# Kernel tuning notes

Hardware: AMD Instinct MI355X
Metric: run time of the kernel (lower is better)

Reference implementation:

```python
import jax, jax.numpy as jnp
import numpy as np

NH, HD, MBS = 32, 64, 16   # num_heads, head_dim, mini_batch_size
BASE_LR = 1.0
ROPE_BASE = 10000.0
EPS = 1e-6


def _rotate_half(x):
    x1, x2 = jnp.split(x, 2, axis=-1)
    return jnp.concatenate((-x2, x1), axis=-1)


def _permute_qk(x):
    B, H, L, D = x.shape
    return x.reshape(B, H, L, D // 2, 2).swapaxes(-1, -2).reshape(B, H, L, D)


def _undo_permute_qk(x):
    B, H, L, D = x.shape
    return x.reshape(B, H, L, 2, D // 2).swapaxes(-1, -2).reshape(B, H, L, D)


def _ln_fwd(x, gamma, beta):
    mu = x.mean(-1, keepdims=True)
    var = x.var(-1, keepdims=True)
    return gamma * ((x - mu) / jnp.sqrt(var + EPS)) + beta


def _ln_fused_l2_bwd(x, target, gamma, beta):
    # grad of 0.5*||LN(x) - target||^2 wrt x, fused
    D = x.shape[-1]
    mu = x.mean(-1, keepdims=True)
    std = jnp.sqrt(x.var(-1, keepdims=True) + EPS)
    x_hat = (x - mu) / std
    y = gamma * x_hat + beta
    g = (y - target) * gamma
    return (D * g - g.sum(-1, keepdims=True) - x_hat * (g * x_hat).sum(-1, keepdims=True)) / (D * std)


def setup_inputs() -> dict:
    key = jax.random.key(0)
    ks = jax.random.split(key, 8)
    B, L, C, OUT = 4, 2048, 2048, 768
    s = 0.02
    return {
        "hidden_states": jax.random.normal(ks[0], (B, L, C), jnp.float32),
        "position_ids": jnp.broadcast_to(jnp.arange(L, dtype=jnp.int32)[None], (B, L)),
        "Wq": jax.random.normal(ks[1], (C, C), jnp.float32) * s,
        "Wk": jax.random.normal(ks[2], (C, C), jnp.float32) * s,
        "Wv": jax.random.normal(ks[3], (C, C), jnp.float32) * s,
        "Wo": jax.random.normal(ks[4], (C, OUT), jnp.float32) * s,
        "W1": jax.random.normal(ks[5], (NH, HD, HD), jnp.float32) * s,
        "b1": jnp.zeros((NH, 1, HD), jnp.float32),
        "ttt_lr_weight": jax.random.normal(ks[6], (NH, 1, C), jnp.float32) * s,
        "ttt_lr_bias": jnp.zeros((NH, 1), jnp.float32),
        "learnable_token_idx": jnp.zeros((MBS,), jnp.float32),
        "ttt_norm_weight": jnp.ones((NH, HD), jnp.float32),
        "ttt_norm_bias": jnp.zeros((NH, HD), jnp.float32),
        "post_norm_weight": jnp.ones((C,), jnp.float32),
        "post_norm_bias": jnp.zeros((C,), jnp.float32),
    }


def reference(hidden_states, position_ids, Wq, Wk, Wv, Wo, W1, b1,
              ttt_lr_weight, ttt_lr_bias, learnable_token_idx,
              ttt_norm_weight, ttt_norm_bias, post_norm_weight, post_norm_bias):
    B, L, C = hidden_states.shape
    NM = L // MBS
    # QKV projections -> [B, NH, L, HD]
    XQ = (hidden_states @ Wq).reshape(B, L, NH, HD).transpose(0, 2, 1, 3)
    XK = (hidden_states @ Wk).reshape(B, L, NH, HD).transpose(0, 2, 1, 3)
    XV = (hidden_states @ Wv).reshape(B, L, NH, HD).transpose(0, 2, 1, 3)
    # RoPE on positions modulo the mini-batch size
    pos = (position_ids % MBS).astype(jnp.float32)  # [B, L]
    inv_freq = 1.0 / (ROPE_BASE ** (jnp.arange(0, HD, 2, dtype=jnp.float32) / HD))
    freqs = pos[..., None] * inv_freq               # [B, L, HD/2]
    emb = jnp.concatenate((freqs, freqs), axis=-1)  # [B, L, HD]
    cos = jnp.cos(emb)[:, None]                     # [B, 1, L, HD]
    sin = jnp.sin(emb)[:, None]
    XQ, XK = _permute_qk(XQ), _permute_qk(XK)
    XQ = XQ * cos + _rotate_half(XQ) * sin
    XK = XK * cos + _rotate_half(XK) * sin
    XQ, XK = _undo_permute_qk(XQ), _undo_permute_qk(XK)
    # reshape into mini-batches: [B, NH, NM, K, HD]
    X = hidden_states.reshape(B, NM, MBS, C)
    XQ = XQ.reshape(B, NH, NM, MBS, HD)
    XK = XK.reshape(B, NH, NM, MBS, HD)
    XV = XV.reshape(B, NH, NM, MBS, HD)
    # eta: per-token learnable LR gate
    ttt_lr = jax.nn.sigmoid(
        jnp.einsum('bnkc,hdc->bhnkd', X, ttt_lr_weight)
        + ttt_lr_bias.reshape(1, NH, 1, 1, 1))              # [B,NH,NM,K,1]
    ttt_lr_eta = BASE_LR * ttt_lr.transpose(0, 1, 2, 4, 3) / HD  # [B,NH,NM,1,K]
    token_idx = jnp.clip(1.0 / jnp.arange(1, MBS + 1, dtype=jnp.float32)
                         + learnable_token_idx, 0.0, None)
    token_eta = token_idx.reshape(1, 1, 1, MBS, 1)
    eta = token_eta * ttt_lr_eta                            # [B,NH,NM,K,K]
    # TTT-Linear dual-form mini-batch scan
    ln_w = ttt_norm_weight.reshape(1, NH, 1, HD)
    ln_b = ttt_norm_bias.reshape(1, NH, 1, HD)
    W1_0 = jnp.broadcast_to(W1[None], (B, NH, HD, HD))
    b1_0 = jnp.broadcast_to(b1[None], (B, NH, 1, HD))
    tril = jnp.tril(jnp.ones((MBS, MBS), hidden_states.dtype))

    def step(carry, xs):
        W1_s, b1_s = carry
        xq, xk, xv, eta_m = xs                 # [B,NH,K,HD], eta_m [B,NH,K,K]
        Z1 = xk @ W1_s + b1_s
        target = xv - xk
        grad = _ln_fused_l2_bwd(Z1, target, ln_w, ln_b)
        Attn = tril * (xq @ xk.swapaxes(-1, -2))
        b1_bar = b1_s - (tril * eta_m) @ grad
        Z1_bar = xq @ W1_s - (eta_m * Attn) @ grad + b1_bar
        last_eta = eta_m[:, :, -1, :, None]    # [B,NH,K,1]
        W1_new = W1_s - (last_eta * xk).swapaxes(-1, -2) @ grad
        b1_new = b1_s - jnp.sum(last_eta * grad, axis=-2, keepdims=True)
        out = xq + _ln_fwd(Z1_bar, ln_w, ln_b)
        return (W1_new, b1_new), out

    xs = (XQ.transpose(2, 0, 1, 3, 4), XK.transpose(2, 0, 1, 3, 4),
          XV.transpose(2, 0, 1, 3, 4), eta.transpose(2, 0, 1, 3, 4))
    _, outs = jax.lax.scan(step, (W1_0, b1_0), xs)   # [NM,B,NH,K,HD]
    out = outs.transpose(1, 2, 0, 3, 4).reshape(B, NH, L, HD)
    out = out.transpose(0, 2, 1, 3).reshape(B, L, C)
    # post LayerNorm (eps 1e-6) and output projection
    mu = out.mean(-1, keepdims=True)
    var = out.var(-1, keepdims=True)
    out = (out - mu) / jnp.sqrt(var + EPS) * post_norm_weight + post_norm_bias
    return out @ Wo
```

## Files before the change

kernel.cpp:

```cpp
#include <hip/hip_runtime.h>
#include <cstddef>
#include <cstdint>

#define B_DIM   4
#define L_SEQ   2048
#define C_DIM   2048
#define OUT_DIM 768
#define NHEADS  32
#define HDIM    64
#define MBS_    16
#define NMINI   128
#define EPS_    1e-6f

typedef _Float16 half8 __attribute__((ext_vector_type(8)));
typedef float floatx4 __attribute__((ext_vector_type(4)));

__device__ __forceinline__ void glds16(const void* g, void* l) {
    __builtin_amdgcn_global_load_lds(
        (const __attribute__((address_space(1))) uint32_t*)g,
        (__attribute__((address_space(3))) uint32_t*)l, 16, 0, 0);
}

__device__ __forceinline__ void split8(const float4 a, const float4 b,
                                       half8& hi, half8& lo) {
    const float x[8] = {a.x, a.y, a.z, a.w, b.x, b.y, b.z, b.w};
#pragma unroll
    for (int e = 0; e < 8; e++) {
        const _Float16 h = (_Float16)x[e];
        hi[e] = h;
        lo[e] = (_Float16)(x[e] - (float)h);
    }
}

__global__ __launch_bounds__(256)
void gemm_af32(const float* __restrict__ A,
               const _Float16* __restrict__ Bhi, const _Float16* __restrict__ Blo,
               float* __restrict__ Cout, int mode, int doRope)
{
    __shared__ __align__(16) float    sA[4096];
    __shared__ __align__(16) _Float16 sBhi[4096];
    __shared__ __align__(16) _Float16 sBlo[4096];
    const int tid = threadIdx.x;
    const int m0 = blockIdx.y * 128, n0 = blockIdx.x * 128;
    const int K = 2048;

    size_t gA[4]; float* lA[4];
#pragma unroll
    for (int I = 0; I < 4; I++) {
        const int c = I * 256 + tid;
        const int row = c >> 3, seg = (c & 7) ^ (row & 7);
        gA[I] = (size_t)(m0 + row) * K + seg * 4;
        lA[I] = &sA[c * 4];
    }
    size_t gB[2]; _Float16 *lBh[2], *lBl[2];
#pragma unroll
    for (int I = 0; I < 2; I++) {
        const int c = I * 256 + tid;
        const int row = c >> 2, seg = (c & 3) ^ ((row >> 1) & 3);
        gB[I] = (size_t)(n0 + row) * K + seg * 8;
        lBh[I] = &sBhi[c * 8];
        lBl[I] = &sBlo[c * 8];
    }

    const int lane = tid & 63, quad = lane >> 4, lc = lane & 15;
    const int wv = tid >> 6, wm = wv & 1, wn = wv >> 1;
    int offA0[4], offA1[4], offB[4];
#pragma unroll
    for (int i = 0; i < 4; i++) {
        const int rA = wm * 64 + i * 16 + lc;
        offA0[i] = (rA * 8 + ((2 * quad)     ^ (rA & 7))) * 4;
        offA1[i] = (rA * 8 + ((2 * quad + 1) ^ (rA & 7))) * 4;
    }
#pragma unroll
    for (int j = 0; j < 4; j++) {
        const int rB = wn * 64 + j * 16 + lc;
        offB[j] = (rB * 4 + (quad ^ ((rB >> 1) & 3))) * 8;
    }

    floatx4 acc[4][4];
#pragma unroll
    for (int i = 0; i < 4; i++)
#pragma unroll
        for (int j = 0; j < 4; j++) acc[i][j] = (floatx4)0.0f;

    for (int k0 = 0; k0 < K; k0 += 32) {
        __syncthreads();
#pragma unroll
        for (int I = 0; I < 4; I++) glds16(A + gA[I] + k0, lA[I]);
#pragma unroll
        for (int I = 0; I < 2; I++) {
            glds16(Bhi + gB[I] + k0, lBh[I]);
            glds16(Blo + gB[I] + k0, lBl[I]);
        }
        __syncthreads();

        half8 ah[4], al[4], bh[4], bl[4];
#pragma unroll
        for (int i = 0; i < 4; i++) {
            const float4 va = *(const float4*)&sA[offA0[i]];
            const float4 vb = *(const float4*)&sA[offA1[i]];
            split8(va, vb, ah[i], al[i]);
        }
#pragma unroll
        for (int j = 0; j < 4; j++) {
            bh[j] = *(const half8*)&sBhi[offB[j]];
            bl[j] = *(const half8*)&sBlo[offB[j]];
        }
#pragma unroll
        for (int i = 0; i < 4; i++)
#pragma unroll
            for (int j = 0; j < 4; j++) {
                acc[i][j] = __builtin_amdgcn_mfma_f32_16x16x32_f16(ah[i], bh[j], acc[i][j], 0, 0, 0);
                acc[i][j] = __builtin_amdgcn_mfma_f32_16x16x32_f16(ah[i], bl[j], acc[i][j], 0, 0, 0);
                acc[i][j] = __builtin_amdgcn_mfma_f32_16x16x32_f16(al[i], bh[j], acc[i][j], 0, 0, 0);
            }
    }

    float cs[4][4], sn[4][4];
    if (doRope) {
#pragma unroll
        for (int j = 0; j < 4; j++) {
            const int ii = ((j * 16 + lc) & 63) >> 1;
            const float invf = expf(-(float)ii * 0.28782313662425574f);
#pragma unroll
            for (int r = 0; r < 4; r++) {
                const float ang = (float)(quad * 4 + r) * invf;
                sincosf(ang, &sn[j][r], &cs[j][r]);
            }
        }
    }
    const int oddcol = lc & 1;
#pragma unroll
    for (int i = 0; i < 4; i++) {
#pragma unroll
        for (int j = 0; j < 4; j++) {
            floatx4 v = acc[i][j];
            if (doRope) {
#pragma unroll
                for (int r = 0; r < 4; r++) {
                    const float partner = __shfl_xor(v[r], 1);
                    v[r] = v[r] * cs[j][r] + partner * (oddcol ? sn[j][r] : -sn[j][r]);
                }
            }
            const int n = n0 + wn * 64 + j * 16 + lc;
            if (mode == 0) {
                const int h = (n >> 6) & 31, d = n & 63;
#pragma unroll
                for (int r = 0; r < 4; r++) {
                    const int m = m0 + wm * 64 + i * 16 + quad * 4 + r;
                    const int b = m >> 11, li = m & 2047;
                    Cout[((size_t)(b * 32 + h) * 2048 + li) * 64 + d] = v[r];
                }
            } else {
#pragma unroll
                for (int r = 0; r < 4; r++) {
                    const int m = m0 + wm * 64 + i * 16 + quad * 4 + r;
                    Cout[(size_t)m * OUT_DIM + n] = v[r];
                }
            }
        }
    }
}

__global__ __launch_bounds__(256)
void wtrans_kernel(const float* __restrict__ W, _Float16* __restrict__ BThi,
                   _Float16* __restrict__ BTlo, int Nw)
{
    __shared__ float tile[32][33];
    const int t = threadIdx.x, tx = t & 31, ty = t >> 5;
    const int n0 = blockIdx.x * 32, k0 = blockIdx.y * 32;
    const int K = 2048;
#pragma unroll
    for (int r = 0; r < 4; r++)
        tile[ty + r * 8][tx] = W[(size_t)(k0 + ty + r * 8) * Nw + n0 + tx];
    __syncthreads();
#pragma unroll
    for (int r = 0; r < 4; r++) {
        const float val = tile[tx][ty + r * 8];
        const _Float16 hh = (_Float16)val;
        const size_t o = (size_t)(n0 + ty + r * 8) * K + k0 + tx;
        BThi[o] = hh;
        BTlo[o] = (_Float16)(val - (float)hh);
    }
}

__global__ __launch_bounds__(256)
void lr_kernel(const float* __restrict__ hidden, const float* __restrict__ wlr,
               const float* __restrict__ lr_bias, float* __restrict__ lrs)
{
    __shared__ float sRow[2048];
    __shared__ float sPart[32][9];
    const int m = blockIdx.x;
    const int t = threadIdx.x;
    const float* row = hidden + (size_t)m * C_DIM;
#pragma unroll
    for (int j = 0; j < 8; j++) sRow[t + j * 256] = row[t + j * 256];
    __syncthreads();
    const int h = t >> 3, p = t & 7;
    const float* w = wlr + (size_t)h * C_DIM;
    float s = 0.0f;
#pragma unroll 8
    for (int k = 0; k < 64; k++) {
        const int c = k * 32 + p * 4;
        const float4 a = *(const float4*)(sRow + c);
        const float4 b = *(const float4*)(w + c);
        s += a.x * b.x + a.y * b.y + a.z * b.z + a.w * b.w;
    }
    sPart[h][p] = s;
    __syncthreads();
    if (t < 32) {
        float v = 0.0f;
#pragma unroll
        for (int p2 = 0; p2 < 8; p2++) v += sPart[t][p2];
        v += lr_bias[t];
        const float sig = 1.0f / (1.0f + expf(-v));
        lrs[((size_t)(m >> 11) * NHEADS + t) * L_SEQ + (m & 2047)] = sig;
    }
}

__global__ __launch_bounds__(256, 1)
void scan_mfma(const float* __restrict__ XQ, const float* __restrict__ XK,
               float* __restrict__ XVo, const float* __restrict__ LRS,
               const float* __restrict__ W1i, const float* __restrict__ b1i,
               const float* __restrict__ lt, const float* __restrict__ lnw,
               const float* __restrict__ lnb)
{
    __shared__ __align__(16) float sXq[1024];
    __shared__ __align__(16) float sXk[1024];
    __shared__ __align__(16) float sXv[16 * 68];
    __shared__ __align__(16) float sW1T[4096];
    __shared__ __align__(16) float sGt[64 * 36];
    __shared__ __align__(16) float sKt[64 * 36];
    __shared__ __align__(16) float sCf[16 * 36];
    __shared__ __align__(16) float sRed[16 * 8];
    __shared__ float sMu[16], sRstd[16], sG1[16], sG2[16];
    __shared__ float sB1[64], sGam[64], sBet[64];
    __shared__ __align__(16) float sEta[32];
    __shared__ float sTok[16];

    const int bh = blockIdx.x, h = bh & 31;
    const int t = threadIdx.x;
    const int lane = t & 63, q = lane >> 4, lc = lane & 15;
    const int w = t >> 6;
    const int col = w * 16 + lc;
    const int iRow = t >> 4;
    const int c0 = (t & 15) * 4;
    const int cellP = (t & 15) ^ (iRow & 15);

    if (t < 64) { sB1[t] = b1i[h * 64 + t]; sGam[t] = lnw[h * 64 + t]; sBet[t] = lnb[h * 64 + t]; }
    if (t < 16) sTok[t] = fmaxf(1.0f / (float)(t + 1) + lt[t], 0.0f);
    if (t < 32) sEta[t] = 0.0f;
    for (int idx = t; idx < 1024; idx += 256) {
        const int r = idx >> 4, c = 16 + (idx & 15);
        sGt[r * 36 + c] = 0.0f;
        sKt[r * 36 + c] = 0.0f;
    }
    { const int r = t >> 4, c = 16 + (t & 15); sCf[r * 36 + c] = 0.0f; }

    float w1s[4][4];
#pragma unroll
    for (int t4 = 0; t4 < 4; t4++)
#pragma unroll
        for (int r = 0; r < 4; r++)
            w1s[t4][r] = W1i[h * 4096 + (16 * t4 + lc) * 64 + (16 * w + 4 * q + r)];
#pragma unroll
    for (int t4 = 0; t4 < 4; t4++)
#pragma unroll
        for (int r = 0; r < 4; r++) {
            const int nn = 16 * w + 4 * q + r, k = 16 * t4 + lc;
            sW1T[nn * 64 + ((((k >> 2) ^ (nn & 15)) << 2) | (k & 3))] = w1s[t4][r];
        }
    __syncthreads();

    const float tok15 = sTok[15];
    const float gamC = sGam[col], betC = sBet[col];
    float tokR[4];
#pragma unroll
    for (int r = 0; r < 4; r++) tokR[r] = sTok[4 * q + r];

    const size_t base = (size_t)bh * L_SEQ * HDIM;
    const float* xq_g = XQ + base;
    const float* xk_g = XK + base;
    float* xv_g = XVo + base;
    const float* lr_g = LRS + (size_t)bh * L_SEQ;

    float4 cq = *(const float4*)(xq_g + t * 4);
    float4 ck = *(const float4*)(xk_g + t * 4);
    float4 cv = *(const float4*)(xv_g + t * 4);
    float clr = lr_g[t & 15];

    for (int n = 0; n < NMINI; n++) {
        *(float4*)&sXq[iRow * 64 + (cellP << 2)] = cq;
        *(float4*)&sXk[iRow * 64 + (cellP << 2)] = ck;
        *(float4*)&sXv[iRow * 68 + c0] = cv;
        if (t < 16) sEta[t] = clr * (1.0f / 64.0f);
        const int np = (n + 1) & (NMINI - 1);
        const float4 nq = *(const float4*)(xq_g + np * 1024 + t * 4);
        const float4 nk = *(const float4*)(xk_g + np * 1024 + t * 4);
        const float4 nv = *(const float4*)(xv_g + np * 1024 + t * 4);
        const float nlr = lr_g[np * 16 + (t & 15)];
        __syncthreads();

        {
            const float le = tok15 * sEta[iRow];
            sKt[(c0 + 0) * 36 + iRow] = ck.x * le;
            sKt[(c0 + 1) * 36 + iRow] = ck.y * le;
            sKt[(c0 + 2) * 36 + iRow] = ck.z * le;
            sKt[(c0 + 3) * 36 + iRow] = ck.w * le;
        }

        half8 qh[2], ql[2], kh[2], kl[2], wh[2], wl[2];
#pragma unroll
        for (int f = 0; f < 2; f++) {
            const int ca = (8 * f + 2 * q) ^ lc, cb = (8 * f + 2 * q + 1) ^ lc;
            {
                const float4 u0 = *(const float4*)&sXq[lc * 64 + ca * 4];
                const float4 u1 = *(const float4*)&sXq[lc * 64 + cb * 4];
                split8(u0, u1, qh[f], ql[f]);
            }
            {
                const float4 u0 = *(const float4*)&sXk[lc * 64 + ca * 4];
                const float4 u1 = *(const float4*)&sXk[lc * 64 + cb * 4];
                split8(u0, u1, kh[f], kl[f]);
            }
            {
                const int rw = 16 * w + lc;
                const float4 u0 = *(const float4*)&sW1T[rw * 64 + ca * 4];
                const float4 u1 = *(const float4*)&sW1T[rw * 64 + cb * 4];
                split8(u0, u1, wh[f], wl[f]);
            }
        }

        floatx4 z1a = (floatx4)0.0f, zba = (floatx4)0.0f, at = (floatx4)0.0f;
#pragma unroll
        for (int f = 0; f < 2; f++) {
            z1a = __builtin_amdgcn_mfma_f32_16x16x32_f16(kh[f], wh[f], z1a, 0, 0, 0);
            z1a = __builtin_amdgcn_mfma_f32_16x16x32_f16(kh[f], wl[f], z1a, 0, 0, 0);
            z1a = __builtin_amdgcn_mfma_f32_16x16x32_f16(kl[f], wh[f], z1a, 0, 0, 0);
            zba = __builtin_amdgcn_mfma_f32_16x16x32_f16(qh[f], wh[f], zba, 0, 0, 0);
            zba = __builtin_amdgcn_mfma_f32_16x16x32_f16(qh[f], wl[f], zba, 0, 0, 0);
            zba = __builtin_amdgcn_mfma_f32_16x16x32_f16(ql[f], wh[f], zba, 0, 0, 0);
        }
        if (w == 0) {
#pragma unroll
            for (int f = 0; f < 2; f++) {
                at = __builtin_amdgcn_mfma_f32_16x16x32_f16(qh[f], kh[f], at, 0, 0, 0);
                at = __builtin_amdgcn_mfma_f32_16x16x32_f16(qh[f], kl[f], at, 0, 0, 0);
                at = __builtin_amdgcn_mfma_f32_16x16x32_f16(ql[f], kh[f], at, 0, 0, 0);
            }
        }

        const float b1c = sB1[col];
        float z[4], s1[4], s2[4];
#pragma unroll
        for (int r = 0; r < 4; r++) { z[r] = z1a[r] + b1c; s1[r] = z[r]; s2[r] = z[r] * z[r]; }
#pragma unroll
        for (int o = 1; o < 16; o <<= 1)
#pragma unroll
            for (int r = 0; r < 4; r++) { s1[r] += __shfl_xor(s1[r], o); s2[r] += __shfl_xor(s2[r], o); }
        if (lc == 0)
#pragma unroll
            for (int r = 0; r < 4; r++) {
                const int row = 4 * q + r;
                sRed[row * 8 + w] = s1[r];
                sRed[row * 8 + 4 + w] = s2[r];
            }
        __syncthreads();
        if (t < 16) {
            const float4 a = *(const float4*)&sRed[t * 8];
            const float4 b = *(const float4*)&sRed[t * 8 + 4];
            const float mu = (a.x + a.y + a.z + a.w) * (1.0f / 64.0f);
            const float ex2 = (b.x + b.y + b.z + b.w) * (1.0f / 64.0f);
            sMu[t] = mu;
            sRstd[t] = rsqrtf(ex2 - mu * mu + EPS_);
        }
        __syncthreads();

        float gg[4], xh[4];
#pragma unroll
        for (int r = 0; r < 4; r++) {
            const int row = 4 * q + r;
            const float mu = sMu[row], rs = sRstd[row];
            xh[r] = (z[r] - mu) * rs;
            const float xkv = sXk[row * 64 + (((((col >> 2) ^ row) & 15) << 2) | (col & 3))];
            const float tgt = sXv[row * 68 + col] - xkv;
            gg[r] = (gamC * xh[r] + betC - tgt) * gamC;
            s1[r] = gg[r]; s2[r] = gg[r] * xh[r];
        }
#pragma unroll
        for (int o = 1; o < 16; o <<= 1)
#pragma unroll
            for (int r = 0; r < 4; r++) { s1[r] += __shfl_xor(s1[r], o); s2[r] += __shfl_xor(s2[r], o); }
        if (lc == 0)
#pragma unroll
            for (int r = 0; r < 4; r++) {
                const int row = 4 * q + r;
                sRed[row * 8 + w] = s1[r];
                sRed[row * 8 + 4 + w] = s2[r];
            }
        __syncthreads();
        if (t < 16) {
            const float4 a = *(const float4*)&sRed[t * 8];
            const float4 b = *(const float4*)&sRed[t * 8 + 4];
            sG1[t] = a.x + a.y + a.z + a.w;
            sG2[t] = b.x + b.y + b.z + b.w;
        }
        __syncthreads();
#pragma unroll
        for (int r = 0; r < 4; r++) {
            const int row = 4 * q + r;
            const float rs = sRstd[row];
            const float gr = (64.0f * gg[r] - sG1[row] - xh[r] * sG2[row]) * rs * (1.0f / 64.0f);
            sGt[col * 36 + row] = gr;
        }
        if (w == 0) {
            const float ej = sEta[lc];
#pragma unroll
            for (int r = 0; r < 4; r++) {
                const int i = 4 * q + r;
                const float cf = (lc <= i) ? -tokR[r] * ej * (at[r] + 1.0f) : 0.0f;
                sCf[i * 36 + lc] = cf;
            }
        }
        __syncthreads();

        half8 cfh, cfl, gth, gtl;
        {
            const float4 u0 = *(const float4*)&sCf[lc * 36 + 8 * q];
            const float4 u1 = *(const float4*)&sCf[lc * 36 + 8 * q + 4];
            split8(u0, u1, cfh, cfl);
        }
        {
            const int rw = 16 * w + lc;
            const float4 u0 = *(const float4*)&sGt[rw * 36 + 8 * q];
            const float4 u1 = *(const float4*)&sGt[rw * 36 + 8 * q + 4];
            split8(u0, u1, gth, gtl);
        }
        zba = __builtin_amdgcn_mfma_f32_16x16x32_f16(cfh, gth, zba, 0, 0, 0);
        zba = __builtin_amdgcn_mfma_f32_16x16x32_f16(cfh, gtl, zba, 0, 0, 0);
        zba = __builtin_amdgcn_mfma_f32_16x16x32_f16(cfl, gth, zba, 0, 0, 0);
#pragma unroll
        for (int t4 = 0; t4 < 4; t4++) {
            half8 kth, ktl;
            const float4 u0 = *(const float4*)&sKt[(16 * t4 + lc) * 36 + 8 * q];
            const float4 u1 = *(const float4*)&sKt[(16 * t4 + lc) * 36 + 8 * q + 4];
            split8(u0, u1, kth, ktl);
            floatx4 up = (floatx4)0.0f;
            up = __builtin_amdgcn_mfma_f32_16x16x32_f16(gth, kth, up, 0, 0, 0);
            up = __builtin_amdgcn_mfma_f32_16x16x32_f16(gth, ktl, up, 0, 0, 0);
            up = __builtin_amdgcn_mfma_f32_16x16x32_f16(gtl, kth, up, 0, 0, 0);
#pragma unroll
            for (int r = 0; r < 4; r++) w1s[t4][r] -= up[r];
        }

        float z2[4];
#pragma unroll
        for (int r = 0; r < 4; r++) { z2[r] = zba[r] + b1c; s1[r] = z2[r]; s2[r] = z2[r] * z2[r]; }
#pragma unroll
        for (int o = 1; o < 16; o <<= 1)
#pragma unroll
            for (int r = 0; r < 4; r++) { s1[r] += __shfl_xor(s1[r], o); s2[r] += __shfl_xor(s2[r], o); }
        if (lc == 0)
#pragma unroll
            for (int r = 0; r < 4; r++) {
                const int row = 4 * q + r;
                sRed[row * 8 + w] = s1[r];
                sRed[row * 8 + 4 + w] = s2[r];
            }
        __syncthreads();
        if (t < 16) {
            const float4 a = *(const float4*)&sRed[t * 8];
            const float4 b = *(const float4*)&sRed[t * 8 + 4];
            const float mu = (a.x + a.y + a.z + a.w) * (1.0f / 64.0f);
            const float ex2 = (b.x + b.y + b.z + b.w) * (1.0f / 64.0f);
            sMu[t] = mu;
            sRstd[t] = rsqrtf(ex2 - mu * mu + EPS_);
        }
        __syncthreads();

#pragma unroll
        for (int r = 0; r < 4; r++) {
            const int row = 4 * q + r;
            const float mu = sMu[row], rs = sRstd[row];
            const float xqv = sXq[row * 64 + (((((col >> 2) ^ row) & 15) << 2) | (col & 3))];
            xv_g[n * 1024 + row * 64 + col] = xqv + gamC * ((z2[r] - mu) * rs) + betC;
        }

        {
            const float4 e0 = *(const float4*)&sEta[8 * q];
            const float4 e1 = *(const float4*)&sEta[8 * q + 4];
            const float ev[8] = {e0.x, e0.y, e0.z, e0.w, e1.x, e1.y, e1.z, e1.w};
            float p = 0.0f;
#pragma unroll
            for (int jj = 0; jj < 8; jj++)
                p += ((float)gth[jj] + (float)gtl[jj]) * ev[jj];
            p += __shfl_xor(p, 16);
            if (q == 0) sB1[col] -= tok15 * p;
        }

#pragma unroll
        for (int t4 = 0; t4 < 4; t4++)
#pragma unroll
            for (int r = 0; r < 4; r++) {
                const int nn = 16 * w + 4 * q + r, k = 16 * t4 + lc;
                sW1T[nn * 64 + ((((k >> 2) ^ (nn & 15)) << 2) | (k & 3))] = w1s[t4][r];
            }
        __syncthreads();
        cq = nq; ck = nk; cv = nv; clr = nlr;
    }
}

__global__ __launch_bounds__(256)
void postln_kernel(const float* __restrict__ Ob, const float* __restrict__ pnw,
                   const float* __restrict__ pnb, float* __restrict__ XN)
{
    const int m = blockIdx.x;
    const int b = m >> 11, l = m & 2047;
    const int t = threadIdx.x;
    float v[8];
    float s1 = 0.0f, s2 = 0.0f;
    const float* bas = Ob + (size_t)b * NHEADS * L_SEQ * HDIM + (size_t)l * HDIM;
#pragma unroll
    for (int j = 0; j < 8; j++) {
        const int c = t + j * 256;
        const int hh = c >> 6, d = c & 63;
        const float x = bas[(size_t)hh * (L_SEQ * HDIM) + d];
        v[j] = x; s1 += x; s2 += x * x;
    }
#pragma unroll
    for (int o = 1; o < 64; o <<= 1) { s1 += __shfl_xor(s1, o); s2 += __shfl_xor(s2, o); }
    __shared__ float r1[4], r2[4];
    const int w = t >> 6;
    if ((t & 63) == 0) { r1[w] = s1; r2[w] = s2; }
    __syncthreads();
    s1 = r1[0] + r1[1] + r1[2] + r1[3];
    s2 = r2[0] + r2[1] + r2[2] + r2[3];
    const float mu = s1 * (1.0f / 2048.0f);
    const float var = s2 * (1.0f / 2048.0f) - mu * mu;
    const float rstd = rsqrtf(var + EPS_);
    float* o = XN + (size_t)m * C_DIM;
#pragma unroll
    for (int j = 0; j < 8; j++) {
        const int c = t + j * 256;
        o[c] = (v[j] - mu) * rstd * pnw[c] + pnb[c];
    }
}

extern "C" void kernel_launch(void* const* d_in, const int* in_sizes, int n_in,
                              void* d_out, int out_size, void* d_ws, size_t ws_size,
                              hipStream_t stream)
{
    (void)in_sizes; (void)n_in; (void)out_size;
    const float* hidden  = (const float*)d_in[0];
    const float* Wq      = (const float*)d_in[2];
    const float* Wk      = (const float*)d_in[3];
    const float* Wv      = (const float*)d_in[4];
    const float* Wo      = (const float*)d_in[5];
    const float* W1      = (const float*)d_in[6];
    const float* b1      = (const float*)d_in[7];
    const float* wlr     = (const float*)d_in[8];
    const float* lr_bias = (const float*)d_in[9];
    const float* lt      = (const float*)d_in[10];
    const float* lnw     = (const float*)d_in[11];
    const float* lnb     = (const float*)d_in[12];
    const float* pnw     = (const float*)d_in[13];
    const float* pnb     = (const float*)d_in[14];

    const size_t TEN = (size_t)B_DIM * NHEADS * L_SEQ * HDIM;
    float* XQ  = (float*)d_ws;
    float* XK  = XQ + TEN;
    float* XVo = XK + TEN;
    float* LRS = XVo + TEN;
    const dim3 blk(256);

    _Float16* BThi = (_Float16*)d_out;
    _Float16* BTlo = BThi + (size_t)C_DIM * C_DIM;

    lr_kernel<<<dim3(B_DIM * L_SEQ), blk, 0, stream>>>(hidden, wlr, lr_bias, LRS);

    const float* Wmats[3] = {Wq, Wk, Wv};
    float* outs[3] = {XQ, XK, XVo};
    for (int p = 0; p < 3; p++) {
        wtrans_kernel<<<dim3(64, 64), blk, 0, stream>>>(Wmats[p], BThi, BTlo, C_DIM);
        gemm_af32<<<dim3(16, 64), blk, 0, stream>>>(hidden, BThi, BTlo,
                                                    outs[p], 0, (p < 2) ? 1 : 0);
    }
    scan_mfma<<<dim3(B_DIM * NHEADS), blk, 0, stream>>>(XQ, XK, XVo, LRS,
                                                        W1, b1, lt, lnw, lnb);
    float* XN = XQ;
    _Float16* WThi = (_Float16*)XK;
    _Float16* WTlo = WThi + (size_t)OUT_DIM * C_DIM;
    postln_kernel<<<dim3(B_DIM * L_SEQ), blk, 0, stream>>>(XVo, pnw, pnb, XN);
    wtrans_kernel<<<dim3(24, 64), blk, 0, stream>>>(Wo, WThi, WTlo, OUT_DIM);
    gemm_af32<<<dim3(6, 64), blk, 0, stream>>>(XN, WThi, WTlo,
                                               (float*)d_out, 1, 0);
}
```

Before: 1.488 ms.

## Store pre-split fp16 hi/lo operands in LDS and cut scan barriers

The scan kernel now splits Q, K, W1, gradient, K-transpose and coefficient tiles into fp16 hi/lo pairs once, when writing them to shared memory, so each MFMA operand is read as a half8 with no per-use conversion. Row-wise LayerNorm statistics are reduced redundantly by every thread from per-pass reduction buffers instead of by one 16-thread group, which removes several __syncthreads per mini-batch. Q is double-buffered and the barrier at the end of the iteration is dropped. This trades more LDS traffic and redundant math for fewer barriers, at the risk of races between iterations now that the last barrier is gone.

```diff
diff --git a/kernel.cpp b/kernel.cpp
--- a/kernel.cpp
+++ b/kernel.cpp
@@ -13,6 +13,7 @@
 #define EPS_    1e-6f
 
 typedef _Float16 half8 __attribute__((ext_vector_type(8)));
+typedef _Float16 half4 __attribute__((ext_vector_type(4)));
 typedef float floatx4 __attribute__((ext_vector_type(4)));
 
 __device__ __forceinline__ void glds16(const void* g, void* l) {
@@ -26,6 +27,16 @@
     const float x[8] = {a.x, a.y, a.z, a.w, b.x, b.y, b.z, b.w};
 #pragma unroll
     for (int e = 0; e < 8; e++) {
+        const _Float16 h = (_Float16)x[e];
+        hi[e] = h;
+        lo[e] = (_Float16)(x[e] - (float)h);
+    }
+}
+
+__device__ __forceinline__ void split4(const float4 a, half4& hi, half4& lo) {
+    const float x[4] = {a.x, a.y, a.z, a.w};
+#pragma unroll
+    for (int e = 0; e < 4; e++) {
         const _Float16 h = (_Float16)x[e];
         hi[e] = h;
         lo[e] = (_Float16)(x[e] - (float)h);
@@ -225,18 +236,15 @@
                const float* __restrict__ lt, const float* __restrict__ lnw,
                const float* __restrict__ lnb)
 {
-    __shared__ __align__(16) float sXq[1024];
-    __shared__ __align__(16) float sXk[1024];
-    __shared__ __align__(16) float sXv[16 * 68];
-    __shared__ __align__(16) float sW1T[4096];
-    __shared__ __align__(16) float sGt[64 * 36];
-    __shared__ __align__(16) float sKt[64 * 36];
-    __shared__ __align__(16) float sCf[16 * 36];
-    __shared__ __align__(16) float sRed[16 * 8];
-    __shared__ float sMu[16], sRstd[16], sG1[16], sG2[16];
-    __shared__ float sB1[64], sGam[64], sBet[64];
-    __shared__ __align__(16) float sEta[32];
-    __shared__ float sTok[16];
+    __shared__ __align__(16) _Float16 sXqH[2][1024], sXqL[2][1024];
+    __shared__ __align__(16) _Float16 sXkH[1024], sXkL[1024];
+    __shared__ __align__(16) float    sXv[16 * 68];
+    __shared__ __align__(16) _Float16 sW1H[4096], sW1L[4096];
+    __shared__ __align__(16) _Float16 sGtH[2560], sGtL[2560];
+    __shared__ __align__(16) _Float16 sKtH[2560], sKtL[2560];
+    __shared__ __align__(16) _Float16 sCfH[640],  sCfL[640];
+    __shared__ __align__(16) float sRedA[128], sRedB[128], sRedC[128];
+    __shared__ float sEta[32], sB1[64];
 
     const int bh = blockIdx.x, h = bh & 31;
     const int t = threadIdx.x;
@@ -244,39 +252,41 @@
     const int w = t >> 6;
     const int col = w * 16 + lc;
     const int iRow = t >> 4;
-    const int c0 = (t & 15) * 4;
-    const int cellP = (t & 15) ^ (iRow & 15);
-
-    if (t < 64) { sB1[t] = b1i[h * 64 + t]; sGam[t] = lnw[h * 64 + t]; sBet[t] = lnb[h * 64 + t]; }
-    if (t < 16) sTok[t] = fmaxf(1.0f / (float)(t + 1) + lt[t], 0.0f);
+    const int m = t & 15;
+
+    if (t < 64) sB1[t] = b1i[h * 64 + t];
     if (t < 32) sEta[t] = 0.0f;
-    for (int idx = t; idx < 1024; idx += 256) {
-        const int r = idx >> 4, c = 16 + (idx & 15);
-        sGt[r * 36 + c] = 0.0f;
-        sKt[r * 36 + c] = 0.0f;
-    }
-    { const int r = t >> 4, c = 16 + (t & 15); sCf[r * 36 + c] = 0.0f; }
+    for (int idx = t; idx < 64 * 24; idx += 256) {
+        const int nn = idx / 24, j = 16 + idx % 24;
+        sGtH[nn * 40 + j] = (_Float16)0.0f; sGtL[nn * 40 + j] = (_Float16)0.0f;
+        sKtH[nn * 40 + j] = (_Float16)0.0f; sKtL[nn * 40 + j] = (_Float16)0.0f;
+    }
+    for (int idx = t; idx < 16 * 24; idx += 256) {
+        const int ii = idx / 24, j = 16 + idx % 24;
+        sCfH[ii * 40 + j] = (_Float16)0.0f; sCfL[ii * 40 + j] = (_Float16)0.0f;
+    }
 
     float w1s[4][4];
 #pragma unroll
     for (int t4 = 0; t4 < 4; t4++)
 #pragma unroll
-        for (int r = 0; r < 4; r++)
-            w1s[t4][r] = W1i[h * 4096 + (16 * t4 + lc) * 64 + (16 * w + 4 * q + r)];
-#pragma unroll
-    for (int t4 = 0; t4 < 4; t4++)
-#pragma unroll
         for (int r = 0; r < 4; r++) {
+            const float v = W1i[h * 4096 + (16 * t4 + lc) * 64 + (16 * w + 4 * q + r)];
+            w1s[t4][r] = v;
             const int nn = 16 * w + 4 * q + r, k = 16 * t4 + lc;
-            sW1T[nn * 64 + ((((k >> 2) ^ (nn & 15)) << 2) | (k & 3))] = w1s[t4][r];
-        }
+            const int off = nn * 64 + ((((k >> 3) ^ (nn & 7)) << 3) | (k & 7));
+            const _Float16 hh = (_Float16)v;
+            sW1H[off] = hh; sW1L[off] = (_Float16)(v - (float)hh);
+        }
+
+    const float gamC = lnw[h * 64 + col], betC = lnb[h * 64 + col];
+    float tokR[4];
+#pragma unroll
+    for (int r = 0; r < 4; r++)
+        tokR[r] = fmaxf(1.0f / (float)(4 * q + r + 1) + lt[4 * q + r], 0.0f);
+    const float tok15 = fmaxf(1.0f / 16.0f + lt[15], 0.0f);
+
     __syncthreads();
-
-    const float tok15 = sTok[15];
-    const float gamC = sGam[col], betC = sBet[col];
-    float tokR[4];
-#pragma unroll
-    for (int r = 0; r < 4; r++) tokR[r] = sTok[4 * q + r];
 
     const size_t base = (size_t)bh * L_SEQ * HDIM;
     const float* xq_g = XQ + base;
@@ -287,48 +297,57 @@
     float4 cq = *(const float4*)(xq_g + t * 4);
     float4 ck = *(const float4*)(xk_g + t * 4);
     float4 cv = *(const float4*)(xv_g + t * 4);
-    float clr = lr_g[t & 15];
+    float clr = lr_g[m];
+
+    const int rw = 16 * w + lc;
 
     for (int n = 0; n < NMINI; n++) {
-        *(float4*)&sXq[iRow * 64 + (cellP << 2)] = cq;
-        *(float4*)&sXk[iRow * 64 + (cellP << 2)] = ck;
-        *(float4*)&sXv[iRow * 68 + c0] = cv;
+        const int buf = n & 1;
+        {
+            half4 hq, lq, hk, lk;
+            split4(cq, hq, lq);
+            split4(ck, hk, lk);
+            const int off = iRow * 64 + ((((m >> 1) ^ (iRow & 7)) << 3) | ((m & 1) << 2));
+            *(half4*)&sXqH[buf][off] = hq;
+            *(half4*)&sXqL[buf][off] = lq;
+            *(half4*)&sXkH[off] = hk;
+            *(half4*)&sXkL[off] = lk;
+            *(float4*)&sXv[iRow * 68 + m * 4] = cv;
+        }
         if (t < 16) sEta[t] = clr * (1.0f / 64.0f);
         const int np = (n + 1) & (NMINI - 1);
         const float4 nq = *(const float4*)(xq_g + np * 1024 + t * 4);
         const float4 nk = *(const float4*)(xk_g + np * 1024 + t * 4);
         const float4 nv = *(const float4*)(xv_g + np * 1024 + t * 4);
-        const float nlr = lr_g[np * 16 + (t & 15)];
+        const float nlr = lr_g[np * 16 + m];
         __syncthreads();
 
         {
             const float le = tok15 * sEta[iRow];
-            sKt[(c0 + 0) * 36 + iRow] = ck.x * le;
-            sKt[(c0 + 1) * 36 + iRow] = ck.y * le;
-            sKt[(c0 + 2) * 36 + iRow] = ck.z * le;
-            sKt[(c0 + 3) * 36 + iRow] = ck.w * le;
-        }
+            const float kvv[4] = {ck.x, ck.y, ck.z, ck.w};
+#pragma unroll
+            for (int i2 = 0; i2 < 4; i2++) {
+                const float v = kvv[i2] * le;
+                const _Float16 hh = (_Float16)v;
+                const int o2 = (4 * m + i2) * 40 + iRow;
+                sKtH[o2] = hh; sKtL[o2] = (_Float16)(v - (float)hh);
+            }
+        }
+        const float b1c = sB1[col];
+        const float4 ev0 = *(const float4*)&sEta[8 * q];
+        const float4 ev1 = *(const float4*)&sEta[8 * q + 4];
 
         half8 qh[2], ql[2], kh[2], kl[2], wh[2], wl[2];
 #pragma unroll
         for (int f = 0; f < 2; f++) {
-            const int ca = (8 * f + 2 * q) ^ lc, cb = (8 * f + 2 * q + 1) ^ lc;
-            {
-                const float4 u0 = *(const float4*)&sXq[lc * 64 + ca * 4];
-                const float4 u1 = *(const float4*)&sXq[lc * 64 + cb * 4];
-                split8(u0, u1, qh[f], ql[f]);
-            }
-            {
-                const float4 u0 = *(const float4*)&sXk[lc * 64 + ca * 4];
-                const float4 u1 = *(const float4*)&sXk[lc * 64 + cb * 4];
-                split8(u0, u1, kh[f], kl[f]);
-            }
-            {
-                const int rw = 16 * w + lc;
-                const float4 u0 = *(const float4*)&sW1T[rw * 64 + ca * 4];
-                const float4 u1 = *(const float4*)&sW1T[rw * 64 + cb * 4];
-                split8(u0, u1, wh[f], wl[f]);
-            }
+            const int cx = ((4 * f + q) ^ (lc & 7)) << 3;
+            qh[f] = *(const half8*)&sXqH[buf][lc * 64 + cx];
+            ql[f] = *(const half8*)&sXqL[buf][lc * 64 + cx];
+            kh[f] = *(const half8*)&sXkH[lc * 64 + cx];
+            kl[f] = *(const half8*)&sXkL[lc * 64 + cx];
+            const int cw = ((4 * f + q) ^ (rw & 7)) << 3;
+            wh[f] = *(const half8*)&sW1H[rw * 64 + cw];
+            wl[f] = *(const half8*)&sW1L[rw * 64 + cw];
         }
 
         floatx4 z1a = (floatx4)0.0f, zba = (floatx4)0.0f, at = (floatx4)0.0f;
@@ -342,15 +361,23 @@
             zba = __builtin_amdgcn_mfma_f32_16x16x32_f16(ql[f], wh[f], zba, 0, 0, 0);
         }
         if (w == 0) {
+            const float etaLC = sEta[lc];
 #pragma unroll
             for (int f = 0; f < 2; f++) {
                 at = __builtin_amdgcn_mfma_f32_16x16x32_f16(qh[f], kh[f], at, 0, 0, 0);
                 at = __builtin_amdgcn_mfma_f32_16x16x32_f16(qh[f], kl[f], at, 0, 0, 0);
                 at = __builtin_amdgcn_mfma_f32_16x16x32_f16(ql[f], kh[f], at, 0, 0, 0);
             }
-        }
-
-        const float b1c = sB1[col];
+#pragma unroll
+            for (int r = 0; r < 4; r++) {
+                const int i = 4 * q + r;
+                const float cf = (lc <= i) ? -tokR[r] * etaLC * (at[r] + 1.0f) : 0.0f;
+                const _Float16 hh = (_Float16)cf;
+                sCfH[i * 40 + lc] = hh;
+                sCfL[i * 40 + lc] = (_Float16)(cf - (float)hh);
+            }
+        }
+
         float z[4], s1[4], s2[4];
 #pragma unroll
         for (int r = 0; r < 4; r++) { z[r] = z1a[r] + b1c; s1[r] = z[r]; s2[r] = z[r] * z[r]; }
@@ -361,28 +388,38 @@
         if (lc == 0)
 #pragma unroll
             for (int r = 0; r < 4; r++) {
-                const int row = 4 * q + r;
-                sRed[row * 8 + w] = s1[r];
-                sRed[row * 8 + 4 + w] = s2[r];
+                sRedA[(4 * q + r) * 8 + w] = s1[r];
+                sRedA[(4 * q + r) * 8 + 4 + w] = s2[r];
             }
         __syncthreads();
-        if (t < 16) {
-            const float4 a = *(const float4*)&sRed[t * 8];
-            const float4 b = *(const float4*)&sRed[t * 8 + 4];
+
+        const half8 cfh = *(const half8*)&sCfH[lc * 40 + 8 * q];
+        const half8 cfl = *(const half8*)&sCfL[lc * 40 + 8 * q];
+        half8 kth[4], ktl[4];
+#pragma unroll
+        for (int t4 = 0; t4 < 4; t4++) {
+            kth[t4] = *(const half8*)&sKtH[(16 * t4 + lc) * 40 + 8 * q];
+            ktl[t4] = *(const half8*)&sKtL[(16 * t4 + lc) * 40 + 8 * q];
+        }
+        float muR[4], rsR[4];
+#pragma unroll
+        for (int r = 0; r < 4; r++) {
+            const int row = 4 * q + r;
+            const float4 a = *(const float4*)&sRedA[row * 8];
+            const float4 b = *(const float4*)&sRedA[row * 8 + 4];
             const float mu = (a.x + a.y + a.z + a.w) * (1.0f / 64.0f);
             const float ex2 = (b.x + b.y + b.z + b.w) * (1.0f / 64.0f);
-            sMu[t] = mu;
-            sRstd[t] = rsqrtf(ex2 - mu * mu + EPS_);
-        }
-        __syncthreads();
+            muR[r] = mu;
+            rsR[r] = rsqrtf(ex2 - mu * mu + EPS_);
+        }
 
         float gg[4], xh[4];
 #pragma unroll
         for (int r = 0; r < 4; r++) {
             const int row = 4 * q + r;
-            const float mu = sMu[row], rs = sRstd[row];
-            xh[r] = (z[r] - mu) * rs;
-            const float xkv = sXk[row * 64 + (((((col >> 2) ^ row) & 15) << 2) | (col & 3))];
+            xh[r] = (z[r] - muR[r]) * rsR[r];
+            const int ok = row * 64 + ((((col >> 3) ^ (row & 7)) << 3) | (col & 7));
+            const float xkv = (float)sXkH[ok] + (float)sXkL[ok];
             const float tgt = sXv[row * 68 + col] - xkv;
             gg[r] = (gamC * xh[r] + betC - tgt) * gamC;
             s1[r] = gg[r]; s2[r] = gg[r] * xh[r];
@@ -394,61 +431,35 @@
         if (lc == 0)
 #pragma unroll
             for (int r = 0; r < 4; r++) {
-                const int row = 4 * q + r;
-                sRed[row * 8 + w] = s1[r];
-                sRed[row * 8 + 4 + w] = s2[r];
+                sRedB[(4 * q + r) * 8 + w] = s1[r];
+                sRedB[(4 * q + r) * 8 + 4 + w] = s2[r];
             }
         __syncthreads();
-        if (t < 16) {
-            const float4 a = *(const float4*)&sRed[t * 8];
-            const float4 b = *(const float4*)&sRed[t * 8 + 4];
-            sG1[t] = a.x + a.y + a.z + a.w;
-            sG2[t] = b.x + b.y + b.z + b.w;
-        }
-        __syncthreads();
+
 #pragma unroll
         for (int r = 0; r < 4; r++) {
             const int row = 4 * q + r;
-            const float rs = sRstd[row];
-            const float gr = (64.0f * gg[r] - sG1[row] - xh[r] * sG2[row]) * rs * (1.0f / 64.0f);
-            sGt[col * 36 + row] = gr;
-        }
-        if (w == 0) {
-            const float ej = sEta[lc];
-#pragma unroll
-            for (int r = 0; r < 4; r++) {
-                const int i = 4 * q + r;
-                const float cf = (lc <= i) ? -tokR[r] * ej * (at[r] + 1.0f) : 0.0f;
-                sCf[i * 36 + lc] = cf;
-            }
-        }
-        __syncthreads();
-
-        half8 cfh, cfl, gth, gtl;
-        {
-            const float4 u0 = *(const float4*)&sCf[lc * 36 + 8 * q];
-            const float4 u1 = *(const float4*)&sCf[lc * 36 + 8 * q + 4];
-            split8(u0, u1, cfh, cfl);
-        }
-        {
-            const int rw = 16 * w + lc;
-            const float4 u0 = *(const float4*)&sGt[rw * 36 + 8 * q];
-            const float4 u1 = *(const float4*)&sGt[rw * 36 + 8 * q + 4];
-            split8(u0, u1, gth, gtl);
-        }
+            const float4 a = *(const float4*)&sRedB[row * 8];
+            const float4 b = *(const float4*)&sRedB[row * 8 + 4];
+            const float G1 = a.x + a.y + a.z + a.w;
+            const float G2 = b.x + b.y + b.z + b.w;
+            const float gr = (64.0f * gg[r] - G1 - xh[r] * G2) * rsR[r] * (1.0f / 64.0f);
+            const _Float16 hh = (_Float16)gr;
+            sGtH[col * 40 + row] = hh;
+            sGtL[col * 40 + row] = (_Float16)(gr - (float)hh);
+        }
+        const half8 gth = *(const half8*)&sGtH[rw * 40 + 8 * q];
+        const half8 gtl = *(const half8*)&sGtL[rw * 40 + 8 * q];
+
         zba = __builtin_amdgcn_mfma_f32_16x16x32_f16(cfh, gth, zba, 0, 0, 0);
         zba = __builtin_amdgcn_mfma_f32_16x16x32_f16(cfh, gtl, zba, 0, 0, 0);
         zba = __builtin_amdgcn_mfma_f32_16x16x32_f16(cfl, gth, zba, 0, 0, 0);
 #pragma unroll
         for (int t4 = 0; t4 < 4; t4++) {
-            half8 kth, ktl;
-            const float4 u0 = *(const float4*)&sKt[(16 * t4 + lc) * 36 + 8 * q];
-            const float4 u1 = *(const float4*)&sKt[(16 * t4 + lc) * 36 + 8 * q + 4];
-            split8(u0, u1, kth, ktl);
             floatx4 up = (floatx4)0.0f;
-            up = __builtin_amdgcn_mfma_f32_16x16x32_f16(gth, kth, up, 0, 0, 0);
-            up = __builtin_amdgcn_mfma_f32_16x16x32_f16(gth, ktl, up, 0, 0, 0);
-            up = __builtin_amdgcn_mfma_f32_16x16x32_f16(gtl, kth, up, 0, 0, 0);
+            up = __builtin_amdgcn_mfma_f32_16x16x32_f16(gth, kth[t4], up, 0, 0, 0);
+            up = __builtin_amdgcn_mfma_f32_16x16x32_f16(gth, ktl[t4], up, 0, 0, 0);
+            up = __builtin_amdgcn_mfma_f32_16x16x32_f16(gtl, kth[t4], up, 0, 0, 0);
 #pragma unroll
             for (int r = 0; r < 4; r++) w1s[t4][r] -= up[r];
         }
@@ -463,37 +474,30 @@
         if (lc == 0)
 #pragma unroll
             for (int r = 0; r < 4; r++) {
-                const int row = 4 * q + r;
-                sRed[row * 8 + w] = s1[r];
-                sRed[row * 8 + 4 + w] = s2[r];
+                sRedC[(4 * q + r) * 8 + w] = s1[r];
+                sRedC[(4 * q + r) * 8 + 4 + w] = s2[r];
             }
         __syncthreads();
-        if (t < 16) {
-            const float4 a = *(const float4*)&sRed[t * 8];
-            const float4 b = *(const float4*)&sRed[t * 8 + 4];
+
+#pragma unroll
+        for (int r = 0; r < 4; r++) {
+            const int row = 4 * q + r;
+            const float4 a = *(const float4*)&sRedC[row * 8];
+            const float4 b = *(const float4*)&sRedC[row * 8 + 4];
             const float mu = (a.x + a.y + a.z + a.w) * (1.0f / 64.0f);
             const float ex2 = (b.x + b.y + b.z + b.w) * (1.0f / 64.0f);
-            sMu[t] = mu;
-            sRstd[t] = rsqrtf(ex2 - mu * mu + EPS_);
-        }
-        __syncthreads();
-
-#pragma unroll
-        for (int r = 0; r < 4; r++) {
-            const int row = 4 * q + r;
-            const float mu = sMu[row], rs = sRstd[row];
-            const float xqv = sXq[row * 64 + (((((col >> 2) ^ row) & 15) << 2) | (col & 3))];
+            const float rs = rsqrtf(ex2 - mu * mu + EPS_);
+            const int oq = row * 64 + ((((col >> 3) ^ (row & 7)) << 3) | (col & 7));
+            const float xqv = (float)sXqH[buf][oq] + (float)sXqL[buf][oq];
             xv_g[n * 1024 + row * 64 + col] = xqv + gamC * ((z2[r] - mu) * rs) + betC;
         }
 
         {
-            const float4 e0 = *(const float4*)&sEta[8 * q];
-            const float4 e1 = *(const float4*)&sEta[8 * q + 4];
-            const float ev[8] = {e0.x, e0.y, e0.z, e0.w, e1.x, e1.y, e1.z, e1.w};
+            const float evv[8] = {ev0.x, ev0.y, ev0.z, ev0.w, ev1.x, ev1.y, ev1.z, ev1.w};
             float p = 0.0f;
 #pragma unroll
             for (int jj = 0; jj < 8; jj++)
-                p += ((float)gth[jj] + (float)gtl[jj]) * ev[jj];
+                p += ((float)gth[jj] + (float)gtl[jj]) * evv[jj];
             p += __shfl_xor(p, 16);
             if (q == 0) sB1[col] -= tok15 * p;
         }
@@ -503,9 +507,11 @@
 #pragma unroll
             for (int r = 0; r < 4; r++) {
                 const int nn = 16 * w + 4 * q + r, k = 16 * t4 + lc;
-                sW1T[nn * 64 + ((((k >> 2) ^ (nn & 15)) << 2) | (k & 3))] = w1s[t4][r];
-            }
-        __syncthreads();
+                const int off = nn * 64 + ((((k >> 3) ^ (nn & 7)) << 3) | (k & 7));
+                const float v = w1s[t4][r];
+                const _Float16 hh = (_Float16)v;
+                sW1H[off] = hh; sW1L[off] = (_Float16)(v - (float)hh);
+            }
         cq = nq; ck = nk; cv = nv; clr = nlr;
     }
 }
```

New measurement: 1.510 ms. About the same (+1.5%).
